# Performance work log

Hardware: AMD Instinct MI355X
Metric: run time of the kernel (lower is better)

## Reference

```python
import jax, jax.numpy as jnp
import numpy as np

DEPTH = 3
B, D, O = 8192, 1024, 1024
HR = 32            # router hidden
HE = 2 * D         # expert hidden
N_NODES = 2 ** DEPTH - 1
N_LEAVES = 2 ** DEPTH


def setup_inputs() -> dict:
    key = jax.random.key(0)
    ks = jax.random.split(key, 9)
    x = jax.random.normal(ks[0], (B, D), dtype=jnp.float32)
    # decision-node router params (stacked over nodes)
    rW1 = jax.random.normal(ks[1], (N_NODES, D, HR), dtype=jnp.float32) * 0.05
    rb1 = jnp.zeros((N_NODES, HR), dtype=jnp.float32)
    rW2 = jax.random.normal(ks[2], (N_NODES, HR, 2), dtype=jnp.float32) * 0.05
    rb2 = jnp.zeros((N_NODES, 2), dtype=jnp.float32)
    # leaf-expert params (stacked over experts)
    eW1 = jax.random.normal(ks[3], (N_LEAVES, D, HE), dtype=jnp.float32) * 0.02
    eb1 = jnp.zeros((N_LEAVES, HE), dtype=jnp.float32)
    eW2 = jax.random.normal(ks[4], (N_LEAVES, HE, O), dtype=jnp.float32) * 0.02
    eb2 = jnp.zeros((N_LEAVES, O), dtype=jnp.float32)
    return {"x": x, "rW1": rW1, "rb1": rb1, "rW2": rW2, "rb2": rb2,
            "eW1": eW1, "eb1": eb1, "eW2": eW2, "eb2": eb2, "top_k": 4}


def _gelu(v):
    return jax.nn.gelu(v, approximate=False)  # torch nn.GELU default = exact erf


def _leaf_probs(x, rW1, rb1, rW2, rb2):
    # all decision nodes batched: [N, B, 2]
    h = _gelu(jnp.einsum('bd,ndh->nbh', x, rW1) + rb1[:, None, :])
    logits = jnp.einsum('nbh,nhc->nbc', h, rW2) + rb2[:, None, :]
    dec = jax.nn.softmax(logits, axis=-1)
    # BFS product of path probabilities, level by level (fixed small loop)
    probs = jnp.ones((x.shape[0], 1), dtype=x.dtype)
    start = 0
    for level in range(DEPTH):
        w = 2 ** level
        dl = dec[start:start + w].transpose(1, 0, 2)       # [B, w, 2]
        probs = (probs[:, :, None] * dl).reshape(x.shape[0], 2 * w)
        start += w
    return probs  # [B, N_LEAVES]


def reference(x, rW1, rb1, rW2, rb2, eW1, eb1, eW2, eb2, top_k):
    leaf_probs = _leaf_probs(x, rW1, rb1, rW2, rb2)
    if top_k is not None and top_k < N_LEAVES:
        vals, idx = jax.lax.top_k(leaf_probs, top_k)       # [B, k]
        sparse = jnp.zeros_like(leaf_probs)
        sparse = sparse.at[jnp.arange(leaf_probs.shape[0])[:, None], idx].set(vals)
        leaf_probs = sparse / (sparse.sum(axis=1, keepdims=True) + 1e-8)
    # all leaf experts, batched (dense weighted sum; skip heuristic is an approximation)
    h = _gelu(jnp.einsum('bd,edh->ebh', x, eW1) + eb1[:, None, :])   # [E, B, HE]
    out = jnp.einsum('ebh,eho->ebo', h, eW2) + eb2[:, None, :]        # [E, B, O]
    y = jnp.einsum('ebo,be->bo', out, leaf_probs)
    return (y, leaf_probs)
```

## Files before the change

### kernel.cpp

```cpp
#include <hip/hip_runtime.h>
#include <hip/hip_bf16.h>
#include <cstdint>

#define B_   8192
#define D_   1024
#define O_   1024
#define HE_  2048
#define NN_  7
#define NL_  8
#define HR_  32
#define RC_  224
#define K3_  3072
#define MTMAX_ 264

typedef __attribute__((ext_vector_type(2))) float f32x2;
typedef __attribute__((ext_vector_type(4))) float f32x4;
typedef __attribute__((ext_vector_type(8))) short bf16x8;
typedef __attribute__((ext_vector_type(4))) unsigned short u16x4;
typedef unsigned short u16;
typedef unsigned int u32;

__device__ __forceinline__ u16 f2bf(float f) {
  __hip_bfloat16 h = __float2bfloat16(f);
  return *reinterpret_cast<u16*>(&h);
}
__device__ __forceinline__ float bf2f(u16 u) {
  u32 v = ((u32)u) << 16;
  return *reinterpret_cast<float*>(&v);
}
__device__ __forceinline__ float gelu_exact(float v) {
  return 0.5f * v * (1.0f + erff(v * 0.7071067811865475f));
}
__device__ __forceinline__ void gload16(const void* g, void* l) {
  __builtin_amdgcn_global_load_lds(
      (const __attribute__((address_space(1))) void*)(uintptr_t)g,
      (__attribute__((address_space(3))) void*)(uintptr_t)l,
      16, 0, 0);
}
#define WAITVM(n) asm volatile("s_waitcnt vmcnt(" #n ")" ::: "memory")
#define WAITLGKM0 do { \
  asm volatile("s_waitcnt lgkmcnt(0)" ::: "memory"); \
  __builtin_amdgcn_sched_barrier(0); } while (0)

__device__ __forceinline__ bool expert_of_tile(
    const int* __restrict__ counts, int mt,
    int& e, int& cnt, long& m0, long& hbase) {
  int tot = 0; e = -1; cnt = 0; int tofe = 0;
#pragma unroll
  for (int f = 0; f < NL_; f++) {
    int c = counts[f];
    int tl = (c + 127) >> 7;
    bool in = (e < 0) && (mt < tot + tl);
    if (in) { e = f; tofe = tot; cnt = c; }
    tot += tl;
  }
  if (e < 0) return false;
  m0 = (long)(mt - tofe) * 128;
  hbase = (long)tofe * 128;
  return true;
}

__global__ __launch_bounds__(256) void build_xbs_kernel(
    const float* __restrict__ in, u16* __restrict__ out) {
  size_t i = ((size_t)blockIdx.x * 256 + threadIdx.x) * 4;
  size_t row = i >> 10;
  int col = (int)(i & 1023);
  f32x4 f = *reinterpret_cast<const f32x4*>(in + i);
  u16x4 hi, lo;
#pragma unroll
  for (int j = 0; j < 4; j++) {
    hi[j] = f2bf(f[j]);
    lo[j] = f2bf(f[j] - bf2f(hi[j]));
  }
  u16* base = out + row * 2048 + col;
  *reinterpret_cast<u16x4*>(base)        = hi;
  *reinterpret_cast<u16x4*>(base + 1024) = lo;
}

__global__ __launch_bounds__(256) void build_wr3_kernel(
    const float* __restrict__ rW1, u16* __restrict__ Wr3) {
  size_t i = ((size_t)blockIdx.x * 256 + threadIdx.x) * 4;
  int c = (int)(i / K3_), k = (int)(i % K3_);
  int j = k >> 10, kk = k & 1023;
  u16x4 o;
  if (c < RC_) {
    int node = c >> 5, h = c & 31;
    const float* src = rW1 + ((size_t)node * 1024 + kk) * HR_ + h;
#pragma unroll
    for (int t = 0; t < 4; t++) {
      float f = src[t * HR_];
      u16 hi = f2bf(f);
      o[t] = (j == 1) ? f2bf(f - bf2f(hi)) : hi;
    }
  } else {
    o[0] = 0; o[1] = 0; o[2] = 0; o[3] = 0;
  }
  *reinterpret_cast<u16x4*>(Wr3 + i) = o;
}

__global__ __launch_bounds__(256) void transpose_cvt_kernel(
    const float* __restrict__ in, u16* __restrict__ out,
    int R, int C, int ldo, long in_estride, long out_estride) {
  __shared__ __attribute__((aligned(16))) float tile[64][65];
  const float* in_e = in + (long)blockIdx.z * in_estride;
  u16* out_e = out + (long)blockIdx.z * out_estride;
  int t = threadIdx.x;
  int r0 = blockIdx.y * 64, c0 = blockIdx.x * 64;
  int cc = t & 63, rbase = t >> 6;
#pragma unroll
  for (int i = 0; i < 16; i++) {
    int rr = rbase + i * 4;
    tile[rr][cc] = in_e[(long)(r0 + rr) * C + c0 + cc];
  }
  __syncthreads();
  int r2 = (t & 31) * 2, cj = t >> 5;
#pragma unroll
  for (int i = 0; i < 8; i++) {
    int c = cj * 8 + i;
    u32 u = (u32)f2bf(tile[r2][c]) | ((u32)f2bf(tile[r2 + 1][c]) << 16);
    *reinterpret_cast<u32*>(out_e + (long)(c0 + c) * ldo + r0 + r2) = u;
  }
}

__global__ __launch_bounds__(256, 2) void router_gemm_kernel(
    const u16* __restrict__ Xbs, const u16* __restrict__ Bm,
    float* __restrict__ H1p) {
  __shared__ __attribute__((aligned(16))) u16 lA[128 * 32];
  __shared__ __attribute__((aligned(16))) u16 lB[128 * 32];
  int tid = threadIdx.x;
  int gid = blockIdx.x;
  int cpx = gridDim.x >> 3;
  gid = (gid & 7) * cpx + (gid >> 3);
  int s = gid >> 7;
  int rem = gid & 127;
  int band = rem >> 4, inb = rem & 15;
  long m0 = (long)(band * 8 + (inb & 7)) * 128;
  long n0 = (long)(inb >> 3) * 128;
  int wid = tid >> 6, lane = tid & 63;
  int wm = wid >> 1, wn = wid & 1;
  f32x4 acc[4][4];
#pragma unroll
  for (int m = 0; m < 4; m++)
#pragma unroll
    for (int n = 0; n < 4; n++) acc[m][n] = (f32x4){0.f, 0.f, 0.f, 0.f};
  int lr = lane & 15, lk = (lane >> 4) * 8;
  int srow = tid >> 2, soff = (tid & 3) * 8;
  const u16* Bb = Bm + n0 * K3_;
  int kbeg = s * 768, kend = kbeg + 768;
  for (int k0 = kbeg; k0 < kend; k0 += 32) {
    int ca = (k0 < 1024) ? k0 : k0 - 1024;
    gload16(Xbs + (m0 + srow) * 2048 + ca + soff, &lA[tid * 8]);
    gload16(Xbs + (m0 + 64 + srow) * 2048 + ca + soff, &lA[(256 + tid) * 8]);
    gload16(Bb + (long)srow * K3_ + k0 + soff, &lB[tid * 8]);
    gload16(Bb + (long)(64 + srow) * K3_ + k0 + soff, &lB[(256 + tid) * 8]);
    __syncthreads();
    bf16x8 af[4], bfr[4];
#pragma unroll
    for (int m = 0; m < 4; m++)
      af[m] = *reinterpret_cast<const bf16x8*>(&lA[(wm * 64 + m * 16 + lr) * 32 + lk]);
#pragma unroll
    for (int n = 0; n < 4; n++)
      bfr[n] = *reinterpret_cast<const bf16x8*>(&lB[(wn * 64 + n * 16 + lr) * 32 + lk]);
#pragma unroll
    for (int m = 0; m < 4; m++)
#pragma unroll
      for (int n = 0; n < 4; n++)
        acc[m][n] = __builtin_amdgcn_mfma_f32_16x16x32_bf16(af[m], bfr[n], acc[m][n], 0, 0, 0);
    __syncthreads();
  }
  int lq = lane >> 4;
#pragma unroll
  for (int m = 0; m < 4; m++)
#pragma unroll
    for (int n = 0; n < 4; n++)
#pragma unroll
      for (int j = 0; j < 4; j++) {
        long row = m0 + wm * 64 + m * 16 + lq * 4 + j;
        long col = n0 + wn * 64 + n * 16 + lr;
        if (col < RC_)
          H1p[((long)s * B_ + row) * RC_ + col] = acc[m][n][j];
      }
}

__global__ __launch_bounds__(256) void router_logits_kernel(
    const float* __restrict__ H1p, const float* __restrict__ rb1,
    const float* __restrict__ rW2, const float* __restrict__ rb2,
    const int* __restrict__ topk_ptr, float* __restrict__ P) {
  int b = blockIdx.x * 256 + threadIdx.x;
  float dec[NN_][2];
#pragma unroll
  for (int n = 0; n < NN_; n++) {
    float l0 = rb2[n * 2], l1 = rb2[n * 2 + 1];
#pragma unroll
    for (int r4 = 0; r4 < HR_; r4 += 4) {
      int c = n * HR_ + r4;
      f32x4 hs = *reinterpret_cast<const f32x4*>(&H1p[((long)0 * B_ + b) * RC_ + c]);
#pragma unroll
      for (int s = 1; s < 4; s++)
        hs += *reinterpret_cast<const f32x4*>(&H1p[((long)s * B_ + b) * RC_ + c]);
      f32x4 bv = *reinterpret_cast<const f32x4*>(rb1 + c);
#pragma unroll
      for (int j = 0; j < 4; j++) {
        float hv = gelu_exact(hs[j] + bv[j]);
        l0 += hv * rW2[(c + j) * 2];
        l1 += hv * rW2[(c + j) * 2 + 1];
      }
    }
    float mx = fmaxf(l0, l1);
    float e0 = expf(l0 - mx), e1 = expf(l1 - mx);
    float sm = e0 + e1;
    dec[n][0] = e0 / sm; dec[n][1] = e1 / sm;
  }
  float v[NL_];
#pragma unroll
  for (int L = 0; L < NL_; L++)
    v[L] = dec[0][L >> 2] * dec[1 + (L >> 2)][(L >> 1) & 1] * dec[3 + (L >> 1)][L & 1];
  int tk = *topk_ptr;
  float p[NL_];
  if (tk < NL_) {
    float s = 0.f;
    bool keep[NL_];
#pragma unroll
    for (int e = 0; e < NL_; e++) {
      int rank = 0;
#pragma unroll
      for (int j = 0; j < NL_; j++)
        rank += ((v[j] > v[e]) || (v[j] == v[e] && j < e)) ? 1 : 0;
      keep[e] = rank < tk;
      if (keep[e]) s += v[e];
    }
    float inv = 1.f / (s + 1e-8f);
#pragma unroll
    for (int e = 0; e < NL_; e++) p[e] = keep[e] ? v[e] * inv : 0.f;
  } else {
#pragma unroll
    for (int e = 0; e < NL_; e++) p[e] = v[e];
  }
#pragma unroll
  for (int e = 0; e < NL_; e++) P[(long)b * NL_ + e] = p[e];
}

__global__ __launch_bounds__(256) void yinit_kernel(
    const float* __restrict__ P, const float* __restrict__ eb2,
    float* __restrict__ y) {
  size_t i = ((size_t)blockIdx.x * 256 + threadIdx.x) * 4;
  size_t row = i >> 10;
  int col = (int)(i & 1023);
  f32x4 s = (f32x4){0.f, 0.f, 0.f, 0.f};
#pragma unroll
  for (int e = 0; e < NL_; e++) {
    float pe = P[row * NL_ + e];
    f32x4 w = *reinterpret_cast<const f32x4*>(eb2 + (size_t)e * O_ + col);
    s += w * pe;
  }
  *reinterpret_cast<f32x4*>(y + i) = s;
}

__global__ __launch_bounds__(256) void compact_kernel(
    const float* __restrict__ P, int* __restrict__ idx,
    int* __restrict__ counts) {
  int e = blockIdx.x, t = threadIdx.x;
  int wave = t >> 6, lane = t & 63;
  __shared__ int wsum[4];
  __shared__ int sbase;
  if (t == 0) sbase = 0;
  __syncthreads();
  for (int c0 = 0; c0 < B_; c0 += 256) {
    int r = c0 + t;
    bool f = P[(long)r * NL_ + e] > 0.f;
    unsigned long long mask = __ballot(f);
    int intra = __popcll(mask & ((1ULL << lane) - 1ULL));
    if (lane == 0) wsum[wave] = __popcll(mask);
    __syncthreads();
    int wpre = 0;
#pragma unroll
    for (int w = 0; w < 4; w++) wpre += (w < wave) ? wsum[w] : 0;
    int tot = wsum[0] + wsum[1] + wsum[2] + wsum[3];
    if (f) idx[(long)e * B_ + sbase + wpre + intra] = r;
    __syncthreads();
    if (t == 0) sbase += tot;
    __syncthreads();
  }
  if (t == 0) counts[e] = sbase;
}

__global__ __launch_bounds__(256, 2) void gemme1_kernel(
    const u16* __restrict__ Xbs, const u16* __restrict__ W1t,
    const float* __restrict__ eb1, const float* __restrict__ P,
    u16* __restrict__ Hall, const int* __restrict__ idx,
    const int* __restrict__ counts) {
  __shared__ __attribute__((aligned(16))) u16 lA[128 * 64];
  __shared__ __attribute__((aligned(16))) u16 lB[128 * 64];
  int tid = threadIdx.x;
  int gid = blockIdx.x;
  int cpx = gridDim.x >> 3;
  gid = (gid & 7) * cpx + (gid >> 3);
  int mt = gid >> 4, nt = gid & 15;
  int e, cnt; long m0, hbase;
  if (!expert_of_tile(counts, mt, e, cnt, m0, hbase)) return;
  long n0 = (long)nt * 128;
  const int* idxe = idx + (long)e * B_;
  int wid = tid >> 6, lane = tid & 63;
  int wm = wid >> 1, wn = wid & 1;
  f32x4 acc[4][4];
#pragma unroll
  for (int m = 0; m < 4; m++)
#pragma unroll
    for (int n = 0; n < 4; n++) acc[m][n] = (f32x4){0.f, 0.f, 0.f, 0.f};
  int lr = lane & 15, lkg = lane >> 4;
  const u16* gA[4]; const u16* gB[4]; int lds_o[4];
  const u16* Bb = W1t + ((size_t)e * HE_ + n0) * D_;
#pragma unroll
  for (int i = 0; i < 4; i++) {
    int sidx = tid + i * 256;
    int r = sidx >> 3, j = sidx & 7;
    int so = ((j ^ (r & 7)) << 3);
    int gi = (m0 + r < cnt) ? idxe[m0 + r] : 0;
    gA[i] = Xbs + (long)gi * 2048 + so;
    gB[i] = Bb + (long)r * D_ + so;
    lds_o[i] = sidx * 8;
  }
  int foA[4][2], foB[4][2];
#pragma unroll
  for (int m = 0; m < 4; m++) {
    int r = wm * 64 + m * 16 + lr;
#pragma unroll
    for (int kk = 0; kk < 2; kk++)
      foA[m][kk] = r * 128 + ((((kk * 4 + lkg) ^ (r & 7))) << 4);
  }
#pragma unroll
  for (int n = 0; n < 4; n++) {
    int r = wn * 64 + n * 16 + lr;
#pragma unroll
    for (int kk = 0; kk < 2; kk++)
      foB[n][kk] = r * 128 + ((((kk * 4 + lkg) ^ (r & 7))) << 4);
  }
  const char* pa = (const char*)lA;
  const char* pb = (const char*)lB;
  for (int k0 = 0; k0 < D_; k0 += 64) {
#pragma unroll
    for (int i = 0; i < 4; i++) gload16(gA[i] + k0, &lA[lds_o[i]]);
#pragma unroll
    for (int i = 0; i < 4; i++) gload16(gB[i] + k0, &lB[lds_o[i]]);
    __syncthreads();
    bf16x8 af[4][2], bfr[4][2];
#pragma unroll
    for (int m = 0; m < 4; m++) {
      af[m][0] = *reinterpret_cast<const bf16x8*>(pa + foA[m][0]);
      af[m][1] = *reinterpret_cast<const bf16x8*>(pa + foA[m][1]);
    }
#pragma unroll
    for (int n = 0; n < 4; n++) {
      bfr[n][0] = *reinterpret_cast<const bf16x8*>(pb + foB[n][0]);
      bfr[n][1] = *reinterpret_cast<const bf16x8*>(pb + foB[n][1]);
    }
#pragma unroll
    for (int m = 0; m < 4; m++)
#pragma unroll
      for (int n = 0; n < 4; n++) {
        acc[m][n] = __builtin_amdgcn_mfma_f32_16x16x32_bf16(af[m][0], bfr[n][0], acc[m][n], 0, 0, 0);
        acc[m][n] = __builtin_amdgcn_mfma_f32_16x16x32_bf16(af[m][1], bfr[n][1], acc[m][n], 0, 0, 0);
      }
    __syncthreads();
  }
  int lq = lane >> 4;
#pragma unroll
  for (int m = 0; m < 4; m++) {
#pragma unroll
    for (int j = 0; j < 4; j++) {
      long lrow = m0 + wm * 64 + m * 16 + lq * 4 + j;
      if (lrow >= cnt) continue;
      int orow = idxe[lrow];
      float pw = P[(long)orow * NL_ + e];
#pragma unroll
      for (int n = 0; n < 4; n++) {
        long col = n0 + wn * 64 + n * 16 + lr;
        float g = gelu_exact(acc[m][n][j] + eb1[(size_t)e * HE_ + col]);
        Hall[(hbase + lrow) * HE_ + col] = f2bf(g * pw);
      }
    }
  }
}

__global__ __launch_bounds__(256, 2) void gemme2_kernel(
    const u16* __restrict__ Hall, const u16* __restrict__ W2t,
    float* __restrict__ y, const int* __restrict__ idx,
    const int* __restrict__ counts) {
  __shared__ __attribute__((aligned(16))) u16 lA[2][128 * 64];
  __shared__ __attribute__((aligned(16))) u16 lB[2][128 * 64];
  int tid = threadIdx.x;
  int gid = blockIdx.x;
  int cpx = gridDim.x >> 3;
  gid = (gid & 7) * cpx + (gid >> 3);
  int mt = gid >> 3, nt = gid & 7;
  int e, cnt; long m0, hbase;
  if (!expert_of_tile(counts, mt, e, cnt, m0, hbase)) return;
  long n0 = (long)nt * 128;
  const int* idxe = idx + (long)e * B_;
  int wid = tid >> 6, lane = tid & 63;
  int wm = wid >> 1, wn = wid & 1;
  f32x4 acc[4][4];
#pragma unroll
  for (int m = 0; m < 4; m++)
#pragma unroll
    for (int n = 0; n < 4; n++) acc[m][n] = (f32x4){0.f, 0.f, 0.f, 0.f};
  int lr = lane & 15, lkg = lane >> 4;
  const u16* Ab = Hall + (hbase + m0) * HE_;
  const u16* Bb = W2t + ((size_t)e * O_ + n0) * HE_;
  const u16* gA[4]; const u16* gB[4]; int lds_o[4];
#pragma unroll
  for (int i = 0; i < 4; i++) {
    int sidx = tid + i * 256;
    int r = sidx >> 3, j = sidx & 7;
    int so = ((j ^ (r & 7)) << 3);
    gA[i] = Ab + (long)r * HE_ + so;
    gB[i] = Bb + (long)r * HE_ + so;
    lds_o[i] = sidx * 8;
  }
  int foA[4][2], foB[4][2];
#pragma unroll
  for (int m = 0; m < 4; m++) {
    int r = wm * 64 + m * 16 + lr;
#pragma unroll
    for (int kk = 0; kk < 2; kk++)
      foA[m][kk] = r * 128 + ((((kk * 4 + lkg) ^ (r & 7))) << 4);
  }
#pragma unroll
  for (int n = 0; n < 4; n++) {
    int r = wn * 64 + n * 16 + lr;
#pragma unroll
    for (int kk = 0; kk < 2; kk++)
      foB[n][kk] = r * 128 + ((((kk * 4 + lkg) ^ (r & 7))) << 4);
  }
#define STAGE2(buf, k0) do { _Pragma("unroll") \
  for (int i_ = 0; i_ < 4; i_++) gload16(gA[i_] + (k0), &lA[buf][lds_o[i_]]); \
  _Pragma("unroll") \
  for (int i_ = 0; i_ < 4; i_++) gload16(gB[i_] + (k0), &lB[buf][lds_o[i_]]); \
  } while (0)
  STAGE2(0, 0);
  int cur = 0;
  constexpr int NT = HE_ / 64;
  for (int t = 0; t < NT; ++t) {
    if (t + 1 < NT) {
      STAGE2(cur ^ 1, (t + 1) * 64);
      WAITVM(8);
    } else {
      WAITVM(0);
    }
    __builtin_amdgcn_s_barrier();
    __builtin_amdgcn_sched_barrier(0);
    const char* pa = (const char*)lA[cur];
    const char* pb = (const char*)lB[cur];
    bf16x8 af[4][2], bfr[4][2];
#pragma unroll
    for (int m = 0; m < 4; m++) {
      af[m][0] = *reinterpret_cast<const bf16x8*>(pa + foA[m][0]);
      af[m][1] = *reinterpret_cast<const bf16x8*>(pa + foA[m][1]);
    }
#pragma unroll
    for (int n = 0; n < 4; n++) {
      bfr[n][0] = *reinterpret_cast<const bf16x8*>(pb + foB[n][0]);
      bfr[n][1] = *reinterpret_cast<const bf16x8*>(pb + foB[n][1]);
    }
    WAITLGKM0;
    __builtin_amdgcn_s_setprio(1);
#pragma unroll
    for (int m = 0; m < 4; m++)
#pragma unroll
      for (int n = 0; n < 4; n++) {
        acc[m][n] = __builtin_amdgcn_mfma_f32_16x16x32_bf16(af[m][0], bfr[n][0], acc[m][n], 0, 0, 0);
        acc[m][n] = __builtin_amdgcn_mfma_f32_16x16x32_bf16(af[m][1], bfr[n][1], acc[m][n], 0, 0, 0);
      }
    __builtin_amdgcn_s_setprio(0);
    __builtin_amdgcn_s_barrier();
    __builtin_amdgcn_sched_barrier(0);
    cur ^= 1;
  }
#undef STAGE2
  int lq = lane >> 4;
#pragma unroll
  for (int m = 0; m < 4; m++) {
#pragma unroll
    for (int j = 0; j < 4; j++) {
      long lrow = m0 + wm * 64 + m * 16 + lq * 4 + j;
      if (lrow >= cnt) continue;
      long orow = idxe[lrow];
#pragma unroll
      for (int n = 0; n < 4; n++) {
        long col = n0 + wn * 64 + n * 16 + lr;
        unsafeAtomicAdd(&y[orow * O_ + col], acc[m][n][j]);
      }
    }
  }
}

extern "C" void kernel_launch(void* const* d_in, const int* in_sizes, int n_in,
                              void* d_out, int out_size, void* d_ws, size_t ws_size,
                              hipStream_t stream) {
  (void)in_sizes; (void)n_in; (void)out_size; (void)ws_size;
  const float* x   = (const float*)d_in[0];
  const float* rW1 = (const float*)d_in[1];
  const float* rb1 = (const float*)d_in[2];
  const float* rW2 = (const float*)d_in[3];
  const float* rb2 = (const float*)d_in[4];
  const float* eW1 = (const float*)d_in[5];
  const float* eb1 = (const float*)d_in[6];
  const float* eW2 = (const float*)d_in[7];
  const float* eb2 = (const float*)d_in[8];
  const int*  topk = (const int*)d_in[9];
  float* y = (float*)d_out;
  float* P = y + (size_t)B_ * O_;

  char* ws = (char*)d_ws;
  u16*  Xbs = (u16*)ws;
  u16*  W1t = (u16*)(ws + 33554432);
  u16*  W2t = (u16*)(ws + 67108864);
  int*  idx    = (int*)(ws + 100663296);
  int*  counts = (int*)(ws + 100925440);
  char* hreg   = ws + 100925952;
  u16*  Hall = (u16*)hreg;
  u16*  Wr3  = (u16*)hreg;
  float* H1p = (float*)(hreg + 2097152);

  build_xbs_kernel<<<(B_ * D_) / 1024, 256, 0, stream>>>(x, Xbs);
  build_wr3_kernel<<<(256 * K3_) / 1024, 256, 0, stream>>>(rW1, Wr3);
  transpose_cvt_kernel<<<dim3(HE_ / 64, D_ / 64, NL_), 256, 0, stream>>>(
      eW1, W1t, D_, HE_, D_, (long)D_ * HE_, (long)HE_ * D_);
  transpose_cvt_kernel<<<dim3(O_ / 64, HE_ / 64, NL_), 256, 0, stream>>>(
      eW2, W2t, HE_, O_, HE_, (long)HE_ * O_, (long)O_ * HE_);
  router_gemm_kernel<<<512, 256, 0, stream>>>(Xbs, Wr3, H1p);
  router_logits_kernel<<<B_ / 256, 256, 0, stream>>>(H1p, rb1, rW2, rb2, topk, P);
  yinit_kernel<<<(B_ * O_) / 1024, 256, 0, stream>>>(P, eb2, y);
  compact_kernel<<<NL_, 256, 0, stream>>>(P, idx, counts);

  gemme1_kernel<<<MTMAX_ * 16, 256, 0, stream>>>(
      Xbs, W1t, eb1, P, Hall, idx, counts);
  gemme2_kernel<<<MTMAX_ * 8, 256, 0, stream>>>(
      Hall, W2t, y, idx, counts);
}
```

Baseline: 638.2 us.

## Double-buffer LDS tiles in expert GEMM1 to overlap global loads with MFMA

Splits the shared-memory A and B tiles of the first expert GEMM into two buffers and prefetches the next K-slice while the current one is consumed, using explicit vmcnt waits and raw barriers in place of __syncthreads. MFMA sections also raise wave priority with s_setprio. The goal is to hide global-to-LDS load latency behind matrix math. LDS use doubles to 64KB per block, which may cut occupancy below the two blocks per CU that the launch bounds request.

```diff
diff --git a/kernel.cpp b/kernel.cpp
--- a/kernel.cpp
+++ b/kernel.cpp
@@ -289,8 +289,8 @@
     const float* __restrict__ eb1, const float* __restrict__ P,
     u16* __restrict__ Hall, const int* __restrict__ idx,
     const int* __restrict__ counts) {
-  __shared__ __attribute__((aligned(16))) u16 lA[128 * 64];
-  __shared__ __attribute__((aligned(16))) u16 lB[128 * 64];
+  __shared__ __attribute__((aligned(16))) u16 lA[2][128 * 64];
+  __shared__ __attribute__((aligned(16))) u16 lB[2][128 * 64];
   int tid = threadIdx.x;
   int gid = blockIdx.x;
   int cpx = gridDim.x >> 3;
@@ -335,14 +335,25 @@
     for (int kk = 0; kk < 2; kk++)
       foB[n][kk] = r * 128 + ((((kk * 4 + lkg) ^ (r & 7))) << 4);
   }
-  const char* pa = (const char*)lA;
-  const char* pb = (const char*)lB;
-  for (int k0 = 0; k0 < D_; k0 += 64) {
-#pragma unroll
-    for (int i = 0; i < 4; i++) gload16(gA[i] + k0, &lA[lds_o[i]]);
-#pragma unroll
-    for (int i = 0; i < 4; i++) gload16(gB[i] + k0, &lB[lds_o[i]]);
-    __syncthreads();
+#define STAGE1(buf, k0) do { _Pragma("unroll") \
+  for (int i_ = 0; i_ < 4; i_++) gload16(gA[i_] + (k0), &lA[buf][lds_o[i_]]); \
+  _Pragma("unroll") \
+  for (int i_ = 0; i_ < 4; i_++) gload16(gB[i_] + (k0), &lB[buf][lds_o[i_]]); \
+  } while (0)
+  STAGE1(0, 0);
+  int cur = 0;
+  constexpr int NT = D_ / 64;
+  for (int t = 0; t < NT; ++t) {
+    if (t + 1 < NT) {
+      STAGE1(cur ^ 1, (t + 1) * 64);
+      WAITVM(8);
+    } else {
+      WAITVM(0);
+    }
+    __builtin_amdgcn_s_barrier();
+    __builtin_amdgcn_sched_barrier(0);
+    const char* pa = (const char*)lA[cur];
+    const char* pb = (const char*)lB[cur];
     bf16x8 af[4][2], bfr[4][2];
 #pragma unroll
     for (int m = 0; m < 4; m++) {
@@ -354,6 +365,8 @@
       bfr[n][0] = *reinterpret_cast<const bf16x8*>(pb + foB[n][0]);
       bfr[n][1] = *reinterpret_cast<const bf16x8*>(pb + foB[n][1]);
     }
+    WAITLGKM0;
+    __builtin_amdgcn_s_setprio(1);
 #pragma unroll
     for (int m = 0; m < 4; m++)
 #pragma unroll
@@ -361,8 +374,12 @@
         acc[m][n] = __builtin_amdgcn_mfma_f32_16x16x32_bf16(af[m][0], bfr[n][0], acc[m][n], 0, 0, 0);
         acc[m][n] = __builtin_amdgcn_mfma_f32_16x16x32_bf16(af[m][1], bfr[n][1], acc[m][n], 0, 0, 0);
       }
-    __syncthreads();
-  }
+    __builtin_amdgcn_s_setprio(0);
+    __builtin_amdgcn_s_barrier();
+    __builtin_amdgcn_sched_barrier(0);
+    cur ^= 1;
+  }
+#undef STAGE1
   int lq = lane >> 4;
 #pragma unroll
   for (int m = 0; m < 4; m++) {
```

Measured after the change: 669.6 us. 1.05x slower.
